# Kernel tuning notes

Hardware: AMD Instinct MI355X
Metric: run time of the kernel (lower is better)

## Reference

```python
import jax, jax.numpy as jnp
import numpy as np

B, N, D, H = 2, 2048, 1024, 16
DH = D // H
SCALE = DH ** -0.5


def setup_inputs() -> dict:
    key = jax.random.key(0)
    ks = jax.random.split(key, 12)
    s = 0.02
    q = jax.random.normal(ks[0], (B, N, D), jnp.float32)
    k = jax.random.normal(ks[1], (B, N, D), jnp.float32)
    v = jax.random.normal(ks[2], (B, N, D), jnp.float32)
    attn_mask = jax.random.randint(ks[3], (B, 1, N, N), 0, 2).astype(bool)
    Wq = jax.random.normal(ks[4], (D, D), jnp.float32) * s
    bq = jnp.zeros((D,), jnp.float32)
    Wk = jax.random.normal(ks[5], (D, D), jnp.float32) * s
    bk = jnp.zeros((D,), jnp.float32)
    Wv = jax.random.normal(ks[6], (D, D), jnp.float32) * s
    bv = jnp.zeros((D,), jnp.float32)
    Wp = jax.random.normal(ks[7], (D, D), jnp.float32) * s
    bp = jnp.zeros((D,), jnp.float32)
    return {"q": q, "k": k, "v": v, "attn_mask": attn_mask,
            "Wq": Wq, "bq": bq, "Wk": Wk, "bk": bk,
            "Wv": Wv, "bv": bv, "Wp": Wp, "bp": bp}


def _heads(x, W, b):
    # (B, N, D) -> (B, H, N, DH)
    Bx, Nx, _ = x.shape
    return (x @ W + b).reshape(Bx, Nx, H, DH).transpose(0, 2, 1, 3)


def reference(q, k, v, attn_mask, Wq, bq, Wk, bk, Wv, bv, Wp, bp):
    qh = _heads(q, Wq, bq)                 # (B, H, Nq, DH)
    kh = _heads(k, Wk, bk)                 # (B, H, Nk, DH)
    vh = _heads(v, Wv, bv)                 # (B, H, Nk, DH)
    attn_raw = jnp.einsum('bhqd,bhkd->bhqk', qh, kh) * SCALE
    attn = jnp.where(attn_mask, -jnp.inf, attn_raw)   # masked_fill(attn_mask, -inf)
    attn = jax.nn.softmax(attn, axis=-1)
    x = jnp.einsum('bhqk,bhkd->bhqd', attn, vh)       # (B, H, Nq, DH)
    x = x.transpose(0, 2, 1, 3).reshape(q.shape[0], q.shape[1], D)
    return x @ Wp + bp
```

## Files before the change

### kernel.cpp

```cpp
#include <hip/hip_runtime.h>
#include <stdint.h>

typedef short bf16x8 __attribute__((ext_vector_type(8)));
typedef float f32x4 __attribute__((ext_vector_type(4)));

#define DEV __device__ __forceinline__

static constexpr int BB = 2, NN = 2048, DD = 1024, HH = 16, DH = 64;
static constexpr float SCLOG2E = 0.18033688011112042f;

static constexpr size_t OFF_PACK   = 1024;
static constexpr size_t PACK_BYTES = (size_t)BB * NN * (NN / 64) * 8ull;
static constexpr size_t OFF_WT     = OFF_PACK + PACK_BYTES;
static constexpr size_t WT_ONE     = (size_t)DD * DD;
static constexpr size_t HEAD_BYTES = (size_t)BB * HH * NN * DH * 2ull;
static constexpr size_t OFF_QH     = OFF_WT + 4 * WT_ONE * 2;
static constexpr size_t OFF_KH     = OFF_QH + HEAD_BYTES;
static constexpr size_t OFF_VT     = OFF_KH + HEAD_BYTES;
static constexpr size_t OFF_X      = OFF_VT + HEAD_BYTES;
static constexpr size_t OFF_KB     = OFF_X + HEAD_BYTES;
static constexpr size_t OFF_VB     = OFF_KB + HEAD_BYTES;
static constexpr size_t NEED_BIG   = OFF_VB + HEAD_BYTES;

DEV unsigned short f2b(float f) {
  unsigned int u = __builtin_bit_cast(unsigned int, f);
  u = (u + 0x7fffu + ((u >> 16) & 1u)) >> 16;
  return (unsigned short)u;
}

#define GLOAD16(gp, lp) __builtin_amdgcn_global_load_lds(                     \
    (const __attribute__((address_space(1))) void*)(gp),                      \
    (__attribute__((address_space(3))) void*)(lp), 16, 0, 0)

__global__ __launch_bounds__(256) void prep(
    const float* W0, const float* W1, const float* W2, const float* W3,
    unsigned short* wt,
    const float* q, const float* k, const float* v,
    unsigned short* qb, unsigned short* kb, unsigned short* vb, int doCvt,
    const void* msrc, unsigned long long* packed) {
  __shared__ unsigned short T[64][72];
  const int id = blockIdx.x, t = threadIdx.x;

  if (id < 1024) {
    int z = id >> 8, local = id & 255;
    int n0 = (local & 15) * 64, k0 = (local >> 4) * 64;
    const float* W = (z == 0) ? W0 : (z == 1) ? W1 : (z == 2) ? W2 : W3;
    unsigned short* dst = wt + (size_t)z * WT_ONE;
    #pragma unroll
    for (int i = 0; i < 4; i++) {
      int row = i * 16 + (t >> 4), col = 4 * (t & 15);
      float4 vv = *(const float4*)&W[(size_t)(k0 + row) * DD + n0 + col];
      T[row][col + 0] = f2b(vv.x); T[row][col + 1] = f2b(vv.y);
      T[row][col + 2] = f2b(vv.z); T[row][col + 3] = f2b(vv.w);
    }
    __syncthreads();
    #pragma unroll
    for (int i = 0; i < 4; i++) {
      int n = i * 16 + (t >> 4), kk = 4 * (t & 15);
      ushort4 o = make_ushort4(T[kk][n], T[kk + 1][n], T[kk + 2][n], T[kk + 3][n]);
      *(ushort4*)&dst[(size_t)(n0 + n) * DD + k0 + kk] = o;
    }
  } else if (id < 7168) {
    if (!doCvt) return;
    int local = id - 1024;
    int z = local / 2048, bx = local % 2048;
    const float* s = (z == 0) ? q : (z == 1) ? k : v;
    unsigned short* d = (z == 0) ? qb : (z == 1) ? kb : vb;
    size_t i = ((size_t)bx * 256 + t) * 8;
    float4 a = *(const float4*)&s[i];
    float4 b2 = *(const float4*)&s[i + 4];
    unsigned short o[8] = {f2b(a.x),  f2b(a.y),  f2b(a.z),  f2b(a.w),
                           f2b(b2.x), f2b(b2.y), f2b(b2.z), f2b(b2.w)};
    *(uint4*)&d[i] = *(const uint4*)o;
  } else {
    unsigned f = 0;
    const unsigned* m32 = (const unsigned*)msrc;
    #pragma unroll
    for (int i = 0; i < 16; i++) {
      unsigned xv = m32[i];
      if (xv != 0u && xv != 1u) f |= 1u;
      if (xv != 0u && xv != 0x3f800000u) f |= 2u;
    }
    int w = (id - 7168) * 256 + t;
    size_t base = (size_t)(w >> 5) * 2048 + (size_t)(w & 31) * 64;
    unsigned long long bits = 0ull;
    if (!(f & 1u)) {
      const int4* p = (const int4*)msrc + (base >> 2);
      #pragma unroll
      for (int c = 0; c < 16; c++) {
        int4 qv = p[c];
        if (qv.x) bits |= 1ull << (4 * c + 0);
        if (qv.y) bits |= 1ull << (4 * c + 1);
        if (qv.z) bits |= 1ull << (4 * c + 2);
        if (qv.w) bits |= 1ull << (4 * c + 3);
      }
    } else if (!(f & 2u)) {
      const float4* p = (const float4*)msrc + (base >> 2);
      #pragma unroll
      for (int c = 0; c < 16; c++) {
        float4 qv = p[c];
        if (qv.x != 0.f) bits |= 1ull << (4 * c + 0);
        if (qv.y != 0.f) bits |= 1ull << (4 * c + 1);
        if (qv.z != 0.f) bits |= 1ull << (4 * c + 2);
        if (qv.w != 0.f) bits |= 1ull << (4 * c + 3);
      }
    } else {
      const uint4* p = (const uint4*)((const char*)msrc + base);
      #pragma unroll
      for (int c = 0; c < 4; c++) {
        uint4 qv = p[c];
        unsigned vals[4] = {qv.x, qv.y, qv.z, qv.w};
        #pragma unroll
        for (int i = 0; i < 4; i++)
          #pragma unroll
          for (int j = 0; j < 4; j++)
            if ((vals[i] >> (8 * j)) & 0xffu) bits |= 1ull << (16 * c + 4 * i + j);
      }
    }
    packed[w] = bits;
  }
}

template <int PROJ>
__global__ __launch_bounds__(256) void gemm_pl(
    const unsigned short* A0, const unsigned short* A1,
    const unsigned short* A2, const unsigned short* Wt,
    const float* b0, const float* b1, const float* b2, const float* b3,
    unsigned short* dQ, unsigned short* dK, unsigned short* dVt, float* out) {
  __shared__ unsigned short Al[3][128 * 32];
  __shared__ unsigned short Bl[3][128 * 32];
  const int t = threadIdx.x;
  const int w = t >> 6, l = t & 63, lr = l & 15, lg = l >> 4;
  const int wm = (w >> 1) * 64, wn = (w & 1) * 64;

  const int wg = blockIdx.x;
  const int chunk = wg & 7, local = wg >> 3;
  const int colBlk = local >> 2, rowBlk = chunk * 4 + (local & 3);
  const int m0 = rowBlk * 128, n0 = colBlk * 128;
  const int z = PROJ ? 3 : (n0 >> 10);
  const int n0z = PROJ ? n0 : (n0 & 1023);
  const unsigned short* Asrc = PROJ ? A0 : (z == 0 ? A0 : (z == 1 ? A1 : A2));
  const unsigned short* Bsrc = Wt + (size_t)z * WT_ONE;
  const float* bias = PROJ ? b3 : (z == 0 ? b0 : (z == 1 ? b1 : b2));

  const unsigned short* aP =
      Asrc + (size_t)(m0 + w * 32 + (l >> 2)) * DD + (l & 3) * 8;
  const unsigned short* bP =
      Bsrc + (size_t)(n0z + w * 32 + (l >> 2)) * DD + (l & 3) * 8;

  f32x4 acc[4][4];
  #pragma unroll
  for (int i = 0; i < 4; i++)
    #pragma unroll
    for (int j = 0; j < 4; j++) acc[i][j] = (f32x4){0.f, 0.f, 0.f, 0.f};

  auto STAGE = [&](int k0, int buf) {
    GLOAD16(aP + k0,           &Al[buf][(w * 32) * 32]);
    GLOAD16(aP + k0 + 16 * DD, &Al[buf][(w * 32 + 16) * 32]);
    GLOAD16(bP + k0,           &Bl[buf][(w * 32) * 32]);
    GLOAD16(bP + k0 + 16 * DD, &Bl[buf][(w * 32 + 16) * 32]);
  };

  STAGE(0, 0);
  STAGE(32, 1);
  int bcur = 0, bnext = 2;
  for (int it = 0; it < DD / 32; ++it) {
    if (it + 2 < DD / 32) {
      STAGE((it + 2) * 32, bnext);
      asm volatile("s_waitcnt vmcnt(8)" ::: "memory");
    } else if (it + 2 == DD / 32) {
      asm volatile("s_waitcnt vmcnt(4)" ::: "memory");
    } else {
      asm volatile("s_waitcnt vmcnt(0)" ::: "memory");
    }
    __builtin_amdgcn_s_barrier();

    bf16x8 af[4], bfr[4];
    #pragma unroll
    for (int mi = 0; mi < 4; mi++)
      af[mi] = *(const bf16x8*)&Al[bcur][(wm + mi * 16 + lr) * 32 + lg * 8];
    #pragma unroll
    for (int ni = 0; ni < 4; ni++)
      bfr[ni] = *(const bf16x8*)&Bl[bcur][(wn + ni * 16 + lr) * 32 + lg * 8];
    #pragma unroll
    for (int mi = 0; mi < 4; mi++)
      #pragma unroll
      for (int ni = 0; ni < 4; ni++)
        acc[mi][ni] = __builtin_amdgcn_mfma_f32_16x16x32_bf16(
            af[mi], bfr[ni], acc[mi][ni], 0, 0, 0);
    __builtin_amdgcn_s_barrier();
    bcur = (bcur == 2) ? 0 : bcur + 1;
    bnext = (bnext == 2) ? 0 : bnext + 1;
  }

  const float scl = (!PROJ && z == 0) ? SCLOG2E : 1.0f;
  #pragma unroll
  for (int mi = 0; mi < 4; mi++) {
    #pragma unroll
    for (int ni = 0; ni < 4; ni++) {
      int col = n0z + wn + ni * 16 + lr;
      float bv = bias[col];
      int h = col >> 6, dh = col & 63;
      int mbase = m0 + wm + mi * 16 + lg * 4;
      if (PROJ) {
        #pragma unroll
        for (int r = 0; r < 4; r++)
          out[(size_t)(mbase + r) * DD + col] = acc[mi][ni][r] + bv;
      } else if (z == 2) {
        int bq = mbase >> 11, n = mbase & 2047;
        unsigned short o4[4];
        #pragma unroll
        for (int r = 0; r < 4; r++) o4[r] = f2b(acc[mi][ni][r] + bv);
        *(ushort4*)&dVt[(((size_t)(bq * HH + h)) * DH + dh) * NN + n] =
            *(const ushort4*)o4;
      } else {
        unsigned short* dst = (z == 0) ? dQ : dK;
        #pragma unroll
        for (int r = 0; r < 4; r++) {
          int m = mbase + r;
          int bq = m >> 11, n = m & 2047;
          dst[(((size_t)(bq * HH + h)) * NN + n) * DH + dh] =
              f2b((acc[mi][ni][r] + bv) * scl);
        }
      }
    }
  }
}

__global__ __launch_bounds__(256) void gemm_qkv_f32(
    const float* A0, const float* A1, const float* A2,
    const unsigned short* Wt,
    const float* b0, const float* b1, const float* b2,
    unsigned short* dQ, unsigned short* dK, unsigned short* dVt) {
  __shared__ unsigned short Al[128 * 32];
  __shared__ unsigned short Bl[128 * 32];
  const int t = threadIdx.x, z = blockIdx.z;
  const int m0 = blockIdx.y * 128, n0 = blockIdx.x * 128;
  const unsigned short* Bsrc = Wt + (size_t)z * WT_ONE;
  const float* Af = (z == 0) ? A0 : (z == 1) ? A1 : A2;
  const float* bias = (z == 0) ? b0 : (z == 1) ? b1 : b2;
  const int w = t >> 6, l = t & 63, lr = l & 15, lg = l >> 4;
  const int wm = (w >> 1) * 64, wn = (w & 1) * 64;

  f32x4 acc[4][4];
  #pragma unroll
  for (int i = 0; i < 4; i++)
    #pragma unroll
    for (int j = 0; j < 4; j++) acc[i][j] = (f32x4){0.f, 0.f, 0.f, 0.f};

  for (int k0 = 0; k0 < DD; k0 += 32) {
    __syncthreads();
    #pragma unroll
    for (int i = 0; i < 4; i++) {
      int row = i * 32 + (t >> 3), kk = 4 * (t & 7);
      float4 vv = *(const float4*)&Af[(size_t)(m0 + row) * DD + k0 + kk];
      ushort4 o4 = make_ushort4(f2b(vv.x), f2b(vv.y), f2b(vv.z), f2b(vv.w));
      *(ushort4*)&Al[row * 32 + kk] = o4;
    }
    #pragma unroll
    for (int c = 0; c < 2; c++)
      GLOAD16(&Bsrc[(size_t)(n0 + w * 32 + c * 16 + (l >> 2)) * DD + k0 + (l & 3) * 8],
              &Bl[(w * 32 + c * 16) * 32]);
    __syncthreads();

    bf16x8 af[4], bfr[4];
    #pragma unroll
    for (int mi = 0; mi < 4; mi++)
      af[mi] = *(const bf16x8*)&Al[(wm + mi * 16 + lr) * 32 + lg * 8];
    #pragma unroll
    for (int ni = 0; ni < 4; ni++)
      bfr[ni] = *(const bf16x8*)&Bl[(wn + ni * 16 + lr) * 32 + lg * 8];
    #pragma unroll
    for (int mi = 0; mi < 4; mi++)
      #pragma unroll
      for (int ni = 0; ni < 4; ni++)
        acc[mi][ni] = __builtin_amdgcn_mfma_f32_16x16x32_bf16(
            af[mi], bfr[ni], acc[mi][ni], 0, 0, 0);
  }

  const float scl = (z == 0) ? SCLOG2E : 1.0f;
  #pragma unroll
  for (int mi = 0; mi < 4; mi++) {
    #pragma unroll
    for (int ni = 0; ni < 4; ni++) {
      int col = n0 + wn + ni * 16 + lr;
      float bv = bias[col];
      int h = col >> 6, dh = col & 63;
      int mbase = m0 + wm + mi * 16 + lg * 4;
      if (z == 2) {
        int bq = mbase >> 11, n = mbase & 2047;
        unsigned short o4[4];
        #pragma unroll
        for (int r = 0; r < 4; r++) o4[r] = f2b(acc[mi][ni][r] + bv);
        *(ushort4*)&dVt[(((size_t)(bq * HH + h)) * DH + dh) * NN + n] =
            *(const ushort4*)o4;
      } else {
        unsigned short* dst = (z == 0) ? dQ : dK;
        #pragma unroll
        for (int r = 0; r < 4; r++) {
          int m = mbase + r;
          int bq = m >> 11, n = m & 2047;
          dst[(((size_t)(bq * HH + h)) * NN + n) * DH + dh] =
              f2b((acc[mi][ni][r] + bv) * scl);
        }
      }
    }
  }
}

__global__ __launch_bounds__(256) void attn_k(
    const unsigned short* qh, const unsigned short* kh,
    const unsigned short* vht, const unsigned long long* packed,
    unsigned short* x) {
  __shared__ __align__(16) unsigned short Kl[64 * 64];
  __shared__ __align__(16) unsigned short Vl[64 * 64];
  __shared__ __align__(16) unsigned short Pl[4][16 * 64];
  char* KlB = (char*)Kl;
  char* VlB = (char*)Vl;
  const int t = threadIdx.x, w = t >> 6, l = t & 63;
  const int lr = l & 15, lg = l >> 4;
  char* PlB = (char*)&Pl[w][0];

  const int id = blockIdx.x;
  const int xcd = id & 7, j = id >> 3;
  const int bhg = xcd * 4 + (j >> 5);
  const int q0 = (j & 31) * 64;
  const int b = bhg >> 4, h = bhg & 15;
  const size_t bh = (size_t)b * HH + h;
  const unsigned short* Q = qh + bh * (size_t)NN * DH;
  const unsigned short* K = kh + bh * (size_t)NN * DH;
  const unsigned short* V = vht + bh * (size_t)NN * DH;
  const int qrow = q0 + w * 16 + lr;
  const unsigned long long* pmrow =
      packed + ((size_t)b * NN + qrow) * (NN / 64);

  bf16x8 qf[2];
  #pragma unroll
  for (int kc = 0; kc < 2; kc++)
    qf[kc] = *(const bf16x8*)&Q[(size_t)qrow * DH + kc * 32 + lg * 8];

  f32x4 o[4];
  #pragma unroll
  for (int f = 0; f < 4; f++) o[f] = (f32x4){0.f, 0.f, 0.f, 0.f};
  float lsum = 0.f;

  const int srow = t >> 2, sc0 = (t & 3) * 32;
  const int swr = (srow & 7) << 4;
  const int swl = (lr & 7) << 4;
  const int sA = srow * 128 + (sc0 ^ swr);
  const int sB = srow * 128 + ((sc0 + 16) ^ swr);

  const unsigned short* kpp = &K[(size_t)srow * DH + sc0 / 2];
  const unsigned short* vpp = &V[(size_t)srow * NN + sc0 / 2];
  uint4 k0r = *(const uint4*)kpp, k1r = *(const uint4*)(kpp + 8);
  uint4 v0r = *(const uint4*)vpp, v1r = *(const uint4*)(vpp + 8);

  for (int kt = 0; kt < NN / 64; kt++) {
    __syncthreads();
    *(uint4*)&KlB[sA] = k0r;
    *(uint4*)&KlB[sB] = k1r;
    *(uint4*)&VlB[sA] = v0r;
    *(uint4*)&VlB[sB] = v1r;
    __syncthreads();
    if (kt + 1 < NN / 64) {
      kpp += 64 * DH;
      vpp += 64;
      k0r = *(const uint4*)kpp;  k1r = *(const uint4*)(kpp + 8);
      v0r = *(const uint4*)vpp;  v1r = *(const uint4*)(vpp + 8);
    }

    unsigned long long mw = pmrow[kt];

    f32x4 sv4[4];
    __builtin_amdgcn_s_setprio(1);
    #pragma unroll
    for (int f = 0; f < 4; f++) {
      f32x4 s = (f32x4){0.f, 0.f, 0.f, 0.f};
      bf16x8 kf0 = *(const bf16x8*)&KlB[(16 * f + lr) * 128 + ((lg * 16) ^ swl)];
      bf16x8 kf1 = *(const bf16x8*)&KlB[(16 * f + lr) * 128 + ((64 + lg * 16) ^ swl)];
      s = __builtin_amdgcn_mfma_f32_16x16x32_bf16(kf0, qf[0], s, 0, 0, 0);
      s = __builtin_amdgcn_mfma_f32_16x16x32_bf16(kf1, qf[1], s, 0, 0, 0);
      sv4[f] = s;
    }
    __builtin_amdgcn_s_setprio(0);

    float part = 0.f;
    #pragma unroll
    for (int f = 0; f < 4; f++) {
      unsigned nib = (unsigned)(mw >> (16 * f + 4 * lg)) & 0xFu;
      float pv[4];
      #pragma unroll
      for (int r = 0; r < 4; r++) {
        float s = ((nib >> r) & 1u) ? -30000.f : sv4[f][r];
        pv[r] = __builtin_amdgcn_exp2f(s);
        part += pv[r];
      }
      unsigned w0, w1;
      asm("v_cvt_pk_bf16_f32 %0, %1, %2" : "=v"(w0) : "v"(pv[0]), "v"(pv[1]));
      asm("v_cvt_pk_bf16_f32 %0, %1, %2" : "=v"(w1) : "v"(pv[2]), "v"(pv[3]));
      *(uint2*)&PlB[lr * 128 + ((f * 32 + lg * 8) ^ swl)] = make_uint2(w0, w1);
    }
    lsum += part;
    asm volatile("s_waitcnt lgkmcnt(0)" ::: "memory");
    __builtin_amdgcn_sched_barrier(0);

    bf16x8 pf0 = *(const bf16x8*)&PlB[lr * 128 + ((lg * 16) ^ swl)];
    bf16x8 pf1 = *(const bf16x8*)&PlB[lr * 128 + ((64 + lg * 16) ^ swl)];
    __builtin_amdgcn_s_setprio(1);
    #pragma unroll
    for (int f = 0; f < 4; f++) {
      bf16x8 vf0 = *(const bf16x8*)&VlB[(16 * f + lr) * 128 + ((lg * 16) ^ swl)];
      o[f] = __builtin_amdgcn_mfma_f32_16x16x32_bf16(vf0, pf0, o[f], 0, 0, 0);
      bf16x8 vf1 = *(const bf16x8*)&VlB[(16 * f + lr) * 128 + ((64 + lg * 16) ^ swl)];
      o[f] = __builtin_amdgcn_mfma_f32_16x16x32_bf16(vf1, pf1, o[f], 0, 0, 0);
    }
    __builtin_amdgcn_s_setprio(0);
  }

  lsum += __shfl_xor(lsum, 16);
  lsum += __shfl_xor(lsum, 32);
  float inv = 1.f / fmaxf(lsum, 1e-30f);
  #pragma unroll
  for (int f = 0; f < 4; f++) {
    unsigned w0, w1;
    float a0 = o[f][0] * inv, a1 = o[f][1] * inv;
    float a2 = o[f][2] * inv, a3 = o[f][3] * inv;
    asm("v_cvt_pk_bf16_f32 %0, %1, %2" : "=v"(w0) : "v"(a0), "v"(a1));
    asm("v_cvt_pk_bf16_f32 %0, %1, %2" : "=v"(w1) : "v"(a2), "v"(a3));
    *(uint2*)&x[((size_t)b * NN + qrow) * DD + h * DH + 16 * f + lg * 4] =
        make_uint2(w0, w1);
  }
}

extern "C" void kernel_launch(void* const* d_in, const int* in_sizes, int n_in,
                              void* d_out, int out_size, void* d_ws, size_t ws_size,
                              hipStream_t stream) {
  const float* q  = (const float*)d_in[0];
  const float* k  = (const float*)d_in[1];
  const float* v  = (const float*)d_in[2];
  const void*  mk = d_in[3];
  const float* Wq = (const float*)d_in[4];
  const float* bq = (const float*)d_in[5];
  const float* Wk = (const float*)d_in[6];
  const float* bk = (const float*)d_in[7];
  const float* Wv = (const float*)d_in[8];
  const float* bv = (const float*)d_in[9];
  const float* Wp = (const float*)d_in[10];
  const float* bp = (const float*)d_in[11];
  float* out = (float*)d_out;
  char* ws = (char*)d_ws;

  unsigned long long* packed = (unsigned long long*)(ws + OFF_PACK);
  unsigned short* wt  = (unsigned short*)(ws + OFF_WT);
  unsigned short* qhp = (unsigned short*)(ws + OFF_QH);
  unsigned short* khp = (unsigned short*)(ws + OFF_KH);
  unsigned short* vht = (unsigned short*)(ws + OFF_VT);
  unsigned short* x   = (unsigned short*)(ws + OFF_X);
  unsigned short* qb  = (unsigned short*)(ws + OFF_X);
  unsigned short* kb  = (unsigned short*)(ws + OFF_KB);
  unsigned short* vb  = (unsigned short*)(ws + OFF_VB);

  const bool big = ws_size >= NEED_BIG;

  prep<<<dim3(7680), 256, 0, stream>>>(Wq, Wk, Wv, Wp, wt, q, k, v,
                                       qb, kb, vb, big ? 1 : 0, mk, packed);
  if (big) {
    gemm_pl<0><<<dim3(768), 256, 0, stream>>>(qb, kb, vb, wt,
                                              bq, bk, bv, bp,
                                              qhp, khp, vht, nullptr);
  } else {
    gemm_qkv_f32<<<dim3(8, 32, 3), 256, 0, stream>>>(q, k, v, wt, bq, bk, bv,
                                                     qhp, khp, vht);
  }
  attn_k<<<dim3(1024), 256, 0, stream>>>(qhp, khp, vht, packed, x);
  gemm_pl<1><<<dim3(256), 256, 0, stream>>>(x, nullptr, nullptr, wt,
                                            bq, bk, bv, bp,
                                            nullptr, nullptr, nullptr, out);
}
```

Before: 166.8 us.

## Process two 16-row query tiles per wave to reuse K/V tiles

Each attention workgroup now handles 128 query rows instead of 64, with every wave computing two independent 16-row query tiles against the same LDS-resident K and V tiles. This halves the grid size and the global K/V traffic and barrier count per query row, and adds a per-wave double P buffer. The mask word for the next key tile is also prefetched a step ahead. The costs are higher register and LDS use, which may reduce occupancy, and fewer workgroups (512) spread across the CUs.

Result: slower. 170.9 us (+2.5%).

```diff
diff --git a/kernel.cpp b/kernel.cpp
--- a/kernel.cpp
+++ b/kernel.cpp
@@ -314,35 +314,44 @@
     unsigned short* x) {
   __shared__ __align__(16) unsigned short Kl[64 * 64];
   __shared__ __align__(16) unsigned short Vl[64 * 64];
-  __shared__ __align__(16) unsigned short Pl[4][16 * 64];
+  __shared__ __align__(16) unsigned short Pl[4][2][16 * 64];
   char* KlB = (char*)Kl;
   char* VlB = (char*)Vl;
   const int t = threadIdx.x, w = t >> 6, l = t & 63;
   const int lr = l & 15, lg = l >> 4;
-  char* PlB = (char*)&Pl[w][0];
+  char* PlA = (char*)&Pl[w][0][0];
+  char* PlBs = (char*)&Pl[w][1][0];
 
   const int id = blockIdx.x;
   const int xcd = id & 7, j = id >> 3;
-  const int bhg = xcd * 4 + (j >> 5);
-  const int q0 = (j & 31) * 64;
+  const int bhg = xcd * 4 + (j >> 4);
+  const int q0 = (j & 15) * 128;
   const int b = bhg >> 4, h = bhg & 15;
   const size_t bh = (size_t)b * HH + h;
   const unsigned short* Q = qh + bh * (size_t)NN * DH;
   const unsigned short* K = kh + bh * (size_t)NN * DH;
   const unsigned short* V = vht + bh * (size_t)NN * DH;
-  const int qrow = q0 + w * 16 + lr;
-  const unsigned long long* pmrow =
-      packed + ((size_t)b * NN + qrow) * (NN / 64);
-
-  bf16x8 qf[2];
-  #pragma unroll
-  for (int kc = 0; kc < 2; kc++)
-    qf[kc] = *(const bf16x8*)&Q[(size_t)qrow * DH + kc * 32 + lg * 8];
-
-  f32x4 o[4];
-  #pragma unroll
-  for (int f = 0; f < 4; f++) o[f] = (f32x4){0.f, 0.f, 0.f, 0.f};
-  float lsum = 0.f;
+  const int qrowA = q0 + w * 16 + lr;
+  const int qrowB = qrowA + 64;
+  const unsigned long long* pmrowA =
+      packed + ((size_t)b * NN + qrowA) * (NN / 64);
+  const unsigned long long* pmrowB =
+      packed + ((size_t)b * NN + qrowB) * (NN / 64);
+
+  bf16x8 qfA[2], qfB[2];
+  #pragma unroll
+  for (int kc = 0; kc < 2; kc++) {
+    qfA[kc] = *(const bf16x8*)&Q[(size_t)qrowA * DH + kc * 32 + lg * 8];
+    qfB[kc] = *(const bf16x8*)&Q[(size_t)qrowB * DH + kc * 32 + lg * 8];
+  }
+
+  f32x4 oA[4], oB[4];
+  #pragma unroll
+  for (int f = 0; f < 4; f++) {
+    oA[f] = (f32x4){0.f, 0.f, 0.f, 0.f};
+    oB[f] = (f32x4){0.f, 0.f, 0.f, 0.f};
+  }
+  float lsumA = 0.f, lsumB = 0.f;
 
   const int srow = t >> 2, sc0 = (t & 3) * 32;
   const int swr = (srow & 7) << 4;
@@ -354,6 +363,7 @@
   const unsigned short* vpp = &V[(size_t)srow * NN + sc0 / 2];
   uint4 k0r = *(const uint4*)kpp, k1r = *(const uint4*)(kpp + 8);
   uint4 v0r = *(const uint4*)vpp, v1r = *(const uint4*)(vpp + 8);
+  unsigned long long mwcA = pmrowA[0], mwcB = pmrowB[0];
 
   for (int kt = 0; kt < NN / 64; kt++) {
     __syncthreads();
@@ -362,72 +372,125 @@
     *(uint4*)&VlB[sA] = v0r;
     *(uint4*)&VlB[sB] = v1r;
     __syncthreads();
+    unsigned long long mwnA = mwcA, mwnB = mwcB;
     if (kt + 1 < NN / 64) {
       kpp += 64 * DH;
       vpp += 64;
       k0r = *(const uint4*)kpp;  k1r = *(const uint4*)(kpp + 8);
       v0r = *(const uint4*)vpp;  v1r = *(const uint4*)(vpp + 8);
-    }
-
-    unsigned long long mw = pmrow[kt];
-
-    f32x4 sv4[4];
+      mwnA = pmrowA[kt + 1];
+      mwnB = pmrowB[kt + 1];
+    }
+
+    f32x4 svA[4], svB[4];
     __builtin_amdgcn_s_setprio(1);
     #pragma unroll
     for (int f = 0; f < 4; f++) {
-      f32x4 s = (f32x4){0.f, 0.f, 0.f, 0.f};
       bf16x8 kf0 = *(const bf16x8*)&KlB[(16 * f + lr) * 128 + ((lg * 16) ^ swl)];
       bf16x8 kf1 = *(const bf16x8*)&KlB[(16 * f + lr) * 128 + ((64 + lg * 16) ^ swl)];
-      s = __builtin_amdgcn_mfma_f32_16x16x32_bf16(kf0, qf[0], s, 0, 0, 0);
-      s = __builtin_amdgcn_mfma_f32_16x16x32_bf16(kf1, qf[1], s, 0, 0, 0);
-      sv4[f] = s;
+      f32x4 sa = (f32x4){0.f, 0.f, 0.f, 0.f};
+      sa = __builtin_amdgcn_mfma_f32_16x16x32_bf16(kf0, qfA[0], sa, 0, 0, 0);
+      sa = __builtin_amdgcn_mfma_f32_16x16x32_bf16(kf1, qfA[1], sa, 0, 0, 0);
+      svA[f] = sa;
+      f32x4 sb = (f32x4){0.f, 0.f, 0.f, 0.f};
+      sb = __builtin_amdgcn_mfma_f32_16x16x32_bf16(kf0, qfB[0], sb, 0, 0, 0);
+      sb = __builtin_amdgcn_mfma_f32_16x16x32_bf16(kf1, qfB[1], sb, 0, 0, 0);
+      svB[f] = sb;
     }
     __builtin_amdgcn_s_setprio(0);
 
-    float part = 0.f;
-    #pragma unroll
-    for (int f = 0; f < 4; f++) {
-      unsigned nib = (unsigned)(mw >> (16 * f + 4 * lg)) & 0xFu;
-      float pv[4];
-      #pragma unroll
-      for (int r = 0; r < 4; r++) {
-        float s = ((nib >> r) & 1u) ? -30000.f : sv4[f][r];
-        pv[r] = __builtin_amdgcn_exp2f(s);
-        part += pv[r];
-      }
-      unsigned w0, w1;
-      asm("v_cvt_pk_bf16_f32 %0, %1, %2" : "=v"(w0) : "v"(pv[0]), "v"(pv[1]));
-      asm("v_cvt_pk_bf16_f32 %0, %1, %2" : "=v"(w1) : "v"(pv[2]), "v"(pv[3]));
-      *(uint2*)&PlB[lr * 128 + ((f * 32 + lg * 8) ^ swl)] = make_uint2(w0, w1);
-    }
-    lsum += part;
-    asm volatile("s_waitcnt lgkmcnt(0)" ::: "memory");
-    __builtin_amdgcn_sched_barrier(0);
-
-    bf16x8 pf0 = *(const bf16x8*)&PlB[lr * 128 + ((lg * 16) ^ swl)];
-    bf16x8 pf1 = *(const bf16x8*)&PlB[lr * 128 + ((64 + lg * 16) ^ swl)];
-    __builtin_amdgcn_s_setprio(1);
-    #pragma unroll
-    for (int f = 0; f < 4; f++) {
-      bf16x8 vf0 = *(const bf16x8*)&VlB[(16 * f + lr) * 128 + ((lg * 16) ^ swl)];
-      o[f] = __builtin_amdgcn_mfma_f32_16x16x32_bf16(vf0, pf0, o[f], 0, 0, 0);
-      bf16x8 vf1 = *(const bf16x8*)&VlB[(16 * f + lr) * 128 + ((64 + lg * 16) ^ swl)];
-      o[f] = __builtin_amdgcn_mfma_f32_16x16x32_bf16(vf1, pf1, o[f], 0, 0, 0);
-    }
-    __builtin_amdgcn_s_setprio(0);
-  }
-
-  lsum += __shfl_xor(lsum, 16);
-  lsum += __shfl_xor(lsum, 32);
-  float inv = 1.f / fmaxf(lsum, 1e-30f);
+    {
+      float part = 0.f;
+      #pragma unroll
+      for (int f = 0; f < 4; f++) {
+        unsigned nib = (unsigned)(mwcA >> (16 * f + 4 * lg)) & 0xFu;
+        float pv[4];
+        #pragma unroll
+        for (int r = 0; r < 4; r++) {
+          float s = ((nib >> r) & 1u) ? -30000.f : svA[f][r];
+          pv[r] = __builtin_amdgcn_exp2f(s);
+          part += pv[r];
+        }
+        unsigned w0, w1;
+        asm("v_cvt_pk_bf16_f32 %0, %1, %2" : "=v"(w0) : "v"(pv[0]), "v"(pv[1]));
+        asm("v_cvt_pk_bf16_f32 %0, %1, %2" : "=v"(w1) : "v"(pv[2]), "v"(pv[3]));
+        *(uint2*)&PlA[lr * 128 + ((f * 32 + lg * 8) ^ swl)] = make_uint2(w0, w1);
+      }
+      lsumA += part;
+      asm volatile("s_waitcnt lgkmcnt(0)" ::: "memory");
+      __builtin_amdgcn_sched_barrier(0);
+
+      bf16x8 pf0 = *(const bf16x8*)&PlA[lr * 128 + ((lg * 16) ^ swl)];
+      bf16x8 pf1 = *(const bf16x8*)&PlA[lr * 128 + ((64 + lg * 16) ^ swl)];
+      __builtin_amdgcn_s_setprio(1);
+      #pragma unroll
+      for (int f = 0; f < 4; f++) {
+        bf16x8 vf0 = *(const bf16x8*)&VlB[(16 * f + lr) * 128 + ((lg * 16) ^ swl)];
+        oA[f] = __builtin_amdgcn_mfma_f32_16x16x32_bf16(vf0, pf0, oA[f], 0, 0, 0);
+        bf16x8 vf1 = *(const bf16x8*)&VlB[(16 * f + lr) * 128 + ((64 + lg * 16) ^ swl)];
+        oA[f] = __builtin_amdgcn_mfma_f32_16x16x32_bf16(vf1, pf1, oA[f], 0, 0, 0);
+      }
+      __builtin_amdgcn_s_setprio(0);
+    }
+
+    {
+      float part = 0.f;
+      #pragma unroll
+      for (int f = 0; f < 4; f++) {
+        unsigned nib = (unsigned)(mwcB >> (16 * f + 4 * lg)) & 0xFu;
+        float pv[4];
+        #pragma unroll
+        for (int r = 0; r < 4; r++) {
+          float s = ((nib >> r) & 1u) ? -30000.f : svB[f][r];
+          pv[r] = __builtin_amdgcn_exp2f(s);
+          part += pv[r];
+        }
+        unsigned w0, w1;
+        asm("v_cvt_pk_bf16_f32 %0, %1, %2" : "=v"(w0) : "v"(pv[0]), "v"(pv[1]));
+        asm("v_cvt_pk_bf16_f32 %0, %1, %2" : "=v"(w1) : "v"(pv[2]), "v"(pv[3]));
+        *(uint2*)&PlBs[lr * 128 + ((f * 32 + lg * 8) ^ swl)] = make_uint2(w0, w1);
+      }
+      lsumB += part;
+      asm volatile("s_waitcnt lgkmcnt(0)" ::: "memory");
+      __builtin_amdgcn_sched_barrier(0);
+
+      bf16x8 pf0 = *(const bf16x8*)&PlBs[lr * 128 + ((lg * 16) ^ swl)];
+      bf16x8 pf1 = *(const bf16x8*)&PlBs[lr * 128 + ((64 + lg * 16) ^ swl)];
+      __builtin_amdgcn_s_setprio(1);
+      #pragma unroll
+      for (int f = 0; f < 4; f++) {
+        bf16x8 vf0 = *(const bf16x8*)&VlB[(16 * f + lr) * 128 + ((lg * 16) ^ swl)];
+        oB[f] = __builtin_amdgcn_mfma_f32_16x16x32_bf16(vf0, pf0, oB[f], 0, 0, 0);
+        bf16x8 vf1 = *(const bf16x8*)&VlB[(16 * f + lr) * 128 + ((64 + lg * 16) ^ swl)];
+        oB[f] = __builtin_amdgcn_mfma_f32_16x16x32_bf16(vf1, pf1, oB[f], 0, 0, 0);
+      }
+      __builtin_amdgcn_s_setprio(0);
+    }
+
+    mwcA = mwnA;
+    mwcB = mwnB;
+  }
+
+  lsumA += __shfl_xor(lsumA, 16);
+  lsumA += __shfl_xor(lsumA, 32);
+  lsumB += __shfl_xor(lsumB, 16);
+  lsumB += __shfl_xor(lsumB, 32);
+  float invA = 1.f / fmaxf(lsumA, 1e-30f);
+  float invB = 1.f / fmaxf(lsumB, 1e-30f);
   #pragma unroll
   for (int f = 0; f < 4; f++) {
     unsigned w0, w1;
-    float a0 = o[f][0] * inv, a1 = o[f][1] * inv;
-    float a2 = o[f][2] * inv, a3 = o[f][3] * inv;
+    float a0 = oA[f][0] * invA, a1 = oA[f][1] * invA;
+    float a2 = oA[f][2] * invA, a3 = oA[f][3] * invA;
     asm("v_cvt_pk_bf16_f32 %0, %1, %2" : "=v"(w0) : "v"(a0), "v"(a1));
     asm("v_cvt_pk_bf16_f32 %0, %1, %2" : "=v"(w1) : "v"(a2), "v"(a3));
-    *(uint2*)&x[((size_t)b * NN + qrow) * DD + h * DH + 16 * f + lg * 4] =
+    *(uint2*)&x[((size_t)b * NN + qrowA) * DD + h * DH + 16 * f + lg * 4] =
+        make_uint2(w0, w1);
+    float c0 = oB[f][0] * invB, c1 = oB[f][1] * invB;
+    float c2 = oB[f][2] * invB, c3 = oB[f][3] * invB;
+    asm("v_cvt_pk_bf16_f32 %0, %1, %2" : "=v"(w0) : "v"(c0), "v"(c1));
+    asm("v_cvt_pk_bf16_f32 %0, %1, %2" : "=v"(w1) : "v"(c2), "v"(c3));
+    *(uint2*)&x[((size_t)b * NN + qrowB) * DD + h * DH + 16 * f + lg * 4] =
         make_uint2(w0, w1);
   }
 }
@@ -472,7 +535,7 @@
     gemm_qkv_f32<<<dim3(8, 32, 3), 256, 0, stream>>>(q, k, v, wt, bq, bk, bv,
                                                      qhp, khp, vht);
   }
-  attn_k<<<dim3(1024), 256, 0, stream>>>(qhp, khp, vht, packed, x);
+  attn_k<<<dim3(512), 256, 0, stream>>>(qhp, khp, vht, packed, x);
   gemm_pl<1><<<dim3(256), 256, 0, stream>>>(x, nullptr, nullptr, wt,
                                             bq, bk, bv, bp,
                                             nullptr, nullptr, nullptr, out);
```
